# Kernel optimization log

Hardware: AMD Instinct MI355X
Metric: run time of the kernel (lower is better)

## Reference

```python
import jax, jax.numpy as jnp
import numpy as np

W, B, C, H = 1600, 4, 1, 900
DENSITY = 0.03          # fraction of valid radar returns per column
DEPTH_MAX = 80.0        # metric depth range


def setup_inputs() -> dict:
    key = jax.random.key(0)
    k1, k2, k3 = jax.random.split(key, 3)
    radar_depth = jax.random.uniform(k1, (W, B, C, H, 1), jnp.float32) * DEPTH_MAX + 1.0
    radar_mask = jax.random.uniform(k2, (W, B, C, H, 1), jnp.float32) < DENSITY
    radar_patches = jnp.where(radar_mask, radar_depth, 0.0)
    # dense monocular depth estimate, strictly positive (all 'valid')
    mde_out_patches = jax.random.uniform(k3, (W, B, C, H, 1), jnp.float32) * DEPTH_MAX + 1.0
    return {"radar_patches": radar_patches, "mde_out_patches": mde_out_patches}


def _process_column(radar_col, mde_col):
    """Sequentially place valid radar depths of one (w,b) column.

    radar_col, mde_col: [H] float (channel 0 of the column).
    Returns radar_gt column [H].
    Matches torch loop: for each valid radar y (ascending), pick mde row with
    closest depth (argmin |mde - d|, first index on ties); if that slot is
    already occupied, search outward offsets +1,-1,+2,-2,... for an empty slot;
    if none found, overwrite the best slot.
    """
    h = radar_col.shape[0]
    ys = jnp.arange(h)
    mde_valid = mde_col != 0
    has_mde = jnp.any(mde_valid)
    BIG = jnp.float32(1e30)
    KBIG = 4 * h  # sentinel key for occupied slots

    def step(col, y):
        depth = radar_col[y]
        valid = depth != 0
        # per-point argmin over valid mde depths
        diffs = jnp.where(mde_valid, jnp.abs(mde_col - depth), BIG)
        best_y = jnp.where(has_mde, jnp.argmin(diffs), y)
        # outward collision search as a vectorized argmin over a priority key:
        #   best_y itself -> 0; offset o, +dy before -dy -> 2*o + (dy<0)
        occ = col != 0
        dy = ys - best_y
        key = 2 * jnp.abs(dy) + (dy < 0).astype(jnp.int32)
        key = jnp.where(ys == best_y, 0, key)
        key = jnp.where(occ, KBIG, key)
        final_y = jnp.argmin(key)
        # all slots occupied -> fall back to best_y (torch overwrites there)
        final_y = jnp.where(key[final_y] >= KBIG, best_y, final_y)
        new_col = jnp.where(valid, col.at[final_y].set(depth), col)
        return new_col, None

    col, _ = jax.lax.scan(step, jnp.zeros(h, radar_col.dtype), ys)
    return col


def reference(radar_patches, mde_out_patches):
    # channel 0 only is read/written, as in the torch code
    radar0 = radar_patches[:, :, 0, :, 0]   # [W, B, H]
    mde0 = mde_out_patches[:, :, 0, :, 0]   # [W, B, H]
    cols = jax.vmap(jax.vmap(_process_column))(radar0, mde0)  # [W, B, H]
    w, b, h = cols.shape
    c = radar_patches.shape[2]
    radar_gt = jnp.zeros((b, c, h, w), radar_patches.dtype)
    radar_gt = radar_gt.at[:, 0].set(jnp.transpose(cols, (1, 2, 0)))  # [B, H, W]
    return radar_gt
```

## Files before the change

kernel.cpp:

```cpp
#include <hip/hip_runtime.h>
#include <cstdint>
#include <cstddef>

#define WDIM 1600
#define BDIM 4
#define HDIM 900
#define NV4  225
#define QCAP 96
#define KBIG (4 * HDIM)
#define BW   6
#define NWAVE 4

#define DPP_MINF(v, ctrl)                                                  \
    v = fminf(v, __int_as_float(__builtin_amdgcn_update_dpp(               \
            __float_as_int(v), __float_as_int(v), ctrl, 0xf, 0xf, false)))
#define DPP_MINI(v, ctrl)                                                  \
    { int _t = __builtin_amdgcn_update_dpp(v, v, ctrl, 0xf, 0xf, false);   \
      v = _t < v ? _t : v; }

__device__ __forceinline__ float rdlane_f(float v, int l) {
    return __int_as_float(__builtin_amdgcn_readlane(__float_as_int(v), l));
}

__global__ __launch_bounds__(64 * NWAVE, 6) void radar_place_kernel(
    const float* __restrict__ radar, const float* __restrict__ mde,
    float* __restrict__ colout , int direct, float* __restrict__ out)
{
    __shared__ __align__(16) float s_col[NWAVE][HDIM];
    __shared__ float s_qd[NWAVE][QCAP];
    __shared__ int   s_qy[NWAVE][QCAP];

    const int wave = threadIdx.x >> 6;
    const int lane = threadIdx.x & 63;
    const int colid = blockIdx.x * NWAVE + wave;
    const float4* mde4   = (const float4*)mde   + (long)colid * NV4;
    const float4* radar4 = (const float4*)radar + (long)colid * NV4;

    float*  colw = s_col[wave];
    float4* col4 = (float4*)colw;
    float*  qd   = s_qd[wave];
    int*    qy   = s_qy[wave];

    const unsigned long long below = (1ull << lane) - 1ull;

    bool hm = false;
#pragma unroll
    for (int c = 0; c < 4; ++c) {
        int i4 = c * 64 + lane;
        if (i4 < NV4) {
            float4 mv = mde4[i4];
            hm = hm || (mv.x != 0.f) || (mv.y != 0.f) || (mv.z != 0.f) || (mv.w != 0.f);
            col4[i4] = mv;
        }
    }
    const bool has_mde = (__ballot(hm) != 0ull);

    int Q = 0;
#pragma unroll
    for (int c = 0; c < 4; ++c) {
        int i4 = c * 64 + lane;
        bool in = (i4 < NV4);
        float4 rv = in ? radar4[i4] : make_float4(0.f, 0.f, 0.f, 0.f);
        unsigned long long b0 = __ballot(rv.x != 0.f);
        unsigned long long b1 = __ballot(rv.y != 0.f);
        unsigned long long b2 = __ballot(rv.z != 0.f);
        unsigned long long b3 = __ballot(rv.w != 0.f);
        int pos = Q + __popcll(b0 & below) + __popcll(b1 & below)
                    + __popcll(b2 & below) + __popcll(b3 & below);
        int y0 = i4 * 4;
        if (rv.x != 0.f) { if (pos < QCAP) { qd[pos] = rv.x; qy[pos] = y0;     } pos++; }
        if (rv.y != 0.f) { if (pos < QCAP) { qd[pos] = rv.y; qy[pos] = y0 + 1; } pos++; }
        if (rv.z != 0.f) { if (pos < QCAP) { qd[pos] = rv.z; qy[pos] = y0 + 2; } pos++; }
        if (rv.w != 0.f) { if (pos < QCAP) { qd[pos] = rv.w; qy[pos] = y0 + 3; } pos++; }
        Q += __popcll(b0) + __popcll(b1) + __popcll(b2) + __popcll(b3);
    }
    if (Q > QCAP) Q = QCAP;

    float m[15];
    if (lane < 60) {
        int yb = lane * 15;
#pragma unroll
        for (int k = 0; k < 15; ++k) {
            float v = colw[yb + k];
            m[k] = (v != 0.f) ? v : 1e30f;
        }
    } else {
#pragma unroll
        for (int k = 0; k < 15; ++k) m[k] = 1e30f;
    }

    float dq_lo = 0.f, dq_hi = 0.f;
    int   qy_lo = 0,   qy_hi = 0;
    if (lane < Q)      { dq_lo = qd[lane];      qy_lo = qy[lane]; }
    if (lane + 64 < Q) { dq_hi = qd[lane + 64]; qy_hi = qy[lane + 64]; }

#pragma unroll
    for (int c = 0; c < 4; ++c) {
        int i4 = c * 64 + lane;
        if (i4 < NV4) col4[i4] = make_float4(0.f, 0.f, 0.f, 0.f);
    }

    int best_lo = 0, best_hi = 0;
    for (int t = 0; t < Q; t += BW) {
        int idxs[BW];
        float d[BW];
#pragma unroll
        for (int i = 0; i < BW; ++i) {
            int idx = t + i; if (idx >= Q) idx = Q - 1;
            idxs[i] = idx;
            if (idx < 64) d[i] = rdlane_f(dq_lo, idx);
            else          d[i] = rdlane_f(dq_hi, idx - 64);
        }
        float bd[BW], bo[BW];
        int bik[BW];
#pragma unroll
        for (int i = 0; i < BW; ++i) { bd[i] = 3.4e38f; bik[i] = 0; }
#pragma unroll
        for (int k = 0; k < 15; ++k) {
            float mm = m[k];
#pragma unroll
            for (int i = 0; i < BW; ++i) {
                float af = fabsf(mm - d[i]);
                if (af < bd[i]) { bd[i] = af; bik[i] = k; }
            }
        }
#pragma unroll
        for (int i = 0; i < BW; ++i) bo[i] = bd[i];
#pragma unroll
        for (int i = 0; i < BW; ++i) DPP_MINF(bd[i], 0x111);
#pragma unroll
        for (int i = 0; i < BW; ++i) DPP_MINF(bd[i], 0x112);
#pragma unroll
        for (int i = 0; i < BW; ++i) DPP_MINF(bd[i], 0x114);
#pragma unroll
        for (int i = 0; i < BW; ++i) DPP_MINF(bd[i], 0x118);
#pragma unroll
        for (int i = 0; i < BW; ++i) DPP_MINF(bd[i], 0x142);
#pragma unroll
        for (int i = 0; i < BW; ++i) DPP_MINF(bd[i], 0x143);
#pragma unroll
        for (int i = 0; i < BW; ++i) {
            int idx = idxs[i];
            int sb;
            if (has_mde) {
                float gm = rdlane_f(bd[i], 63);
                unsigned long long wm = __ballot(bo[i] == gm);
                int win = __ffsll((long long)wm) - 1;
                int kst = __builtin_amdgcn_readlane(bik[i], win);
                sb = win * 15 + kst;
            } else {
                if (idx < 64) sb = __builtin_amdgcn_readlane(qy_lo, idx);
                else          sb = __builtin_amdgcn_readlane(qy_hi, idx - 64);
            }
            if (idx < 64) { if (lane == idx)      best_lo = sb; }
            else          { if (lane == idx - 64) best_hi = sb; }
        }
    }

    unsigned occ = (lane >= 60) ? 0x7FFFu : 0u;
    int fy_lo = 0, fy_hi = 0;

    auto place_one = [&](int sb) -> int {
        int bl = sb / 15, bk = sb - bl * 15;
        unsigned long long bm = __ballot((occ >> bk) & 1u);
        int fy = sb;
        if ((bm >> bl) & 1ull) {
            int ko = 0x7fffffff, kk = 0;
#pragma unroll
            for (int k = 0; k < 15; ++k) {
                int yy = lane * 15 + k;
                int o = (occ >> k) & 1;
                int dy = yy - sb;
                int ad = dy < 0 ? -dy : dy;
                int key = o ? KBIG : (2 * ad + (dy < 0 ? 1 : 0));
                if (key < ko) { ko = key; kk = k; }
            }
            int km = ko;
            DPP_MINI(km, 0x111); DPP_MINI(km, 0x112); DPP_MINI(km, 0x114);
            DPP_MINI(km, 0x118); DPP_MINI(km, 0x142); DPP_MINI(km, 0x143);
            int gkm = __builtin_amdgcn_readlane(km, 63);
            if (gkm < KBIG) {
                unsigned long long wm2 = __ballot(ko == gkm);
                int w2 = __ffsll((long long)wm2) - 1;
                int k2 = __builtin_amdgcn_readlane(kk, w2);
                fy = w2 * 15 + k2;
            }
        }
        int fl2 = fy / 15, fk2 = fy - (fy / 15) * 15;
        if (lane == fl2) occ |= (1u << fk2);
        return fy;
    };

    int Qlo = Q < 64 ? Q : 64;
    for (int q = 0; q < Qlo; ++q) {
        int fy = place_one(__builtin_amdgcn_readlane(best_lo, q));
        if (lane == q) fy_lo = fy;
    }
    for (int q = 64; q < Q; ++q) {
        int fy = place_one(__builtin_amdgcn_readlane(best_hi, q - 64));
        if (lane == q - 64) fy_hi = fy;
    }

    if (lane < Q)      colw[fy_lo] = dq_lo;
    if (lane + 64 < Q) colw[fy_hi] = dq_hi;

    if (direct) {
        int w_ = colid >> 2, b_ = colid & 3;
#pragma unroll
        for (int c = 0; c < 4; ++c) {
            int i4 = c * 64 + lane;
            if (i4 < NV4) {
                float4 v = col4[i4];
                int y = i4 * 4;
                out[((long)(b_ * HDIM + y + 0)) * WDIM + w_] = v.x;
                out[((long)(b_ * HDIM + y + 1)) * WDIM + w_] = v.y;
                out[((long)(b_ * HDIM + y + 2)) * WDIM + w_] = v.z;
                out[((long)(b_ * HDIM + y + 3)) * WDIM + w_] = v.w;
            }
        }
    } else {
        float4* colout4 = (float4*)colout + (long)colid * NV4;
#pragma unroll
        for (int c = 0; c < 4; ++c) {
            int i4 = c * 64 + lane;
            if (i4 < NV4) colout4[i4] = col4[i4];
        }
    }
}

__global__ __launch_bounds__(256) void transpose_kernel(
    const float* __restrict__ colout, float* __restrict__ out)
{
    __shared__ float tile[32][33];
    const int b  = blockIdx.z;
    const int h0 = blockIdx.x * 32;
    const int w0 = blockIdx.y * 32;
    const int tx = threadIdx.x & 31;
    const int ty = threadIdx.x >> 5;
#pragma unroll
    for (int j = 0; j < 4; ++j) {
        int wl = ty + j * 8;
        int w = w0 + wl;
        int h = h0 + tx;
        float v = 0.0f;
        if (h < HDIM && w < WDIM) v = colout[((long)(w * BDIM + b)) * HDIM + h];
        tile[wl][tx] = v;
    }
    __syncthreads();
#pragma unroll
    for (int j = 0; j < 4; ++j) {
        int hl = ty + j * 8;
        int h = h0 + hl;
        int w = w0 + tx;
        if (h < HDIM && w < WDIM)
            out[((long)(b * HDIM + h)) * WDIM + w] = tile[tx][hl];
    }
}

extern "C" void kernel_launch(void* const* d_in, const int* in_sizes, int n_in,
                              void* d_out, int out_size, void* d_ws, size_t ws_size,
                              hipStream_t stream) {
    const float* radar = (const float*)d_in[0];
    const float* mde   = (const float*)d_in[1];
    float* out = (float*)d_out;
    float* ws  = (float*)d_ws;

    const size_t need = (size_t)WDIM * BDIM * HDIM * sizeof(float);
    const int direct = (ws_size < need) ? 1 : 0;

    hipLaunchKernelGGL(radar_place_kernel,
                       dim3(WDIM * BDIM / NWAVE), dim3(64 * NWAVE), 0, stream,
                       radar, mde, ws, direct, out);

    if (!direct) {
        dim3 g((HDIM + 31) / 32, WDIM / 32, BDIM);
        hipLaunchKernelGGL(transpose_kernel, g, dim3(256), 0, stream, ws, out);
    }
}
```

Baseline: 138.7 us.

## Pack lane/slot/y indices, widen argmin batch, hoist has_mde branch

Raises the number of radar points resolved per argmin batch from 6 to 9 and hoists the has_mde test out of the batch loop. Points beyond 64 are now handled one at a time, and the loaded qy array is dropped from the main path. Best and final slots are packed as (lane, k, y) so the per-placement divides by 15 disappear. The occupancy check becomes a single readlane instead of a ballot. Launch bounds rise to 7 blocks per CU, which tightens the register budget while the batch grows, so spills are a risk.

```diff
diff --git a/kernel.cpp b/kernel.cpp
--- a/kernel.cpp
+++ b/kernel.cpp
@@ -8,7 +8,7 @@
 #define NV4  225
 #define QCAP 96
 #define KBIG (4 * HDIM)
-#define BW   6
+#define BW   9
 #define NWAVE 4
 
 #define DPP_MINF(v, ctrl)                                                  \
@@ -22,7 +22,11 @@
     return __int_as_float(__builtin_amdgcn_readlane(__float_as_int(v), l));
 }
 
-__global__ __launch_bounds__(64 * NWAVE, 6) void radar_place_kernel(
+__device__ __forceinline__ int pack_lky(int l, int k) {
+    return (l << 20) | (k << 16) | (l * 15 + k);
+}
+
+__global__ __launch_bounds__(64 * NWAVE, 7) void radar_place_kernel(
     const float* __restrict__ radar, const float* __restrict__ mde,
     float* __restrict__ colout , int direct, float* __restrict__ out)
 {
@@ -90,9 +94,8 @@
     }
 
     float dq_lo = 0.f, dq_hi = 0.f;
-    int   qy_lo = 0,   qy_hi = 0;
-    if (lane < Q)      { dq_lo = qd[lane];      qy_lo = qy[lane]; }
-    if (lane + 64 < Q) { dq_hi = qd[lane + 64]; qy_hi = qy[lane + 64]; }
+    if (lane < Q)      dq_lo = qd[lane];
+    if (lane + 64 < Q) dq_hi = qd[lane + 64];
 
 #pragma unroll
     for (int c = 0; c < 4; ++c) {
@@ -101,76 +104,101 @@
     }
 
     int best_lo = 0, best_hi = 0;
-    for (int t = 0; t < Q; t += BW) {
-        int idxs[BW];
-        float d[BW];
-#pragma unroll
-        for (int i = 0; i < BW; ++i) {
-            int idx = t + i; if (idx >= Q) idx = Q - 1;
-            idxs[i] = idx;
-            if (idx < 64) d[i] = rdlane_f(dq_lo, idx);
-            else          d[i] = rdlane_f(dq_hi, idx - 64);
-        }
-        float bd[BW], bo[BW];
-        int bik[BW];
-#pragma unroll
-        for (int i = 0; i < BW; ++i) { bd[i] = 3.4e38f; bik[i] = 0; }
-#pragma unroll
-        for (int k = 0; k < 15; ++k) {
-            float mm = m[k];
+    const int Qlo = Q < 64 ? Q : 64;
+
+    if (has_mde) {
+        for (int t = 0; t < Qlo; t += BW) {
+            float d[BW];
 #pragma unroll
             for (int i = 0; i < BW; ++i) {
-                float af = fabsf(mm - d[i]);
-                if (af < bd[i]) { bd[i] = af; bik[i] = k; }
-            }
-        }
-#pragma unroll
-        for (int i = 0; i < BW; ++i) bo[i] = bd[i];
-#pragma unroll
-        for (int i = 0; i < BW; ++i) DPP_MINF(bd[i], 0x111);
-#pragma unroll
-        for (int i = 0; i < BW; ++i) DPP_MINF(bd[i], 0x112);
-#pragma unroll
-        for (int i = 0; i < BW; ++i) DPP_MINF(bd[i], 0x114);
-#pragma unroll
-        for (int i = 0; i < BW; ++i) DPP_MINF(bd[i], 0x118);
-#pragma unroll
-        for (int i = 0; i < BW; ++i) DPP_MINF(bd[i], 0x142);
-#pragma unroll
-        for (int i = 0; i < BW; ++i) DPP_MINF(bd[i], 0x143);
-#pragma unroll
-        for (int i = 0; i < BW; ++i) {
-            int idx = idxs[i];
-            int sb;
-            if (has_mde) {
-                float gm = rdlane_f(bd[i], 63);
-                unsigned long long wm = __ballot(bo[i] == gm);
+                int idx = t + i; if (idx >= Qlo) idx = Qlo - 1;
+                d[i] = rdlane_f(dq_lo, idx);
+            }
+            float bd[BW], bo[BW];
+            int bik[BW];
+#pragma unroll
+            for (int i = 0; i < BW; ++i) { bd[i] = 3.4e38f; bik[i] = 0; }
+#pragma unroll
+            for (int k = 0; k < 15; ++k) {
+                float mm = m[k];
+#pragma unroll
+                for (int i = 0; i < BW; ++i) {
+                    float af = fabsf(mm - d[i]);
+                    if (af < bd[i]) { bd[i] = af; bik[i] = k; }
+                }
+            }
+#pragma unroll
+            for (int i = 0; i < BW; ++i) bo[i] = bd[i];
+#pragma unroll
+            for (int i = 0; i < BW; ++i) DPP_MINF(bd[i], 0x111);
+#pragma unroll
+            for (int i = 0; i < BW; ++i) DPP_MINF(bd[i], 0x112);
+#pragma unroll
+            for (int i = 0; i < BW; ++i) DPP_MINF(bd[i], 0x114);
+#pragma unroll
+            for (int i = 0; i < BW; ++i) DPP_MINF(bd[i], 0x118);
+#pragma unroll
+            for (int i = 0; i < BW; ++i) DPP_MINF(bd[i], 0x142);
+#pragma unroll
+            for (int i = 0; i < BW; ++i) DPP_MINF(bd[i], 0x143);
+#pragma unroll
+            for (int i = 0; i < BW; ++i) {
+                int idx = t + i;
+                if (idx < Qlo) {
+                    float gm = rdlane_f(bd[i], 63);
+                    unsigned long long wm = __ballot(bo[i] == gm);
+                    int win = __ffsll((long long)wm) - 1;
+                    int kst = __builtin_amdgcn_readlane(bik[i], win);
+                    int pk = pack_lky(win, kst);
+                    if (lane == idx) best_lo = pk;
+                }
+            }
+        }
+        if (Q > 64) {
+            for (int t = 64; t < Q; t += 1) {
+                float d0 = rdlane_f(dq_hi, t - 64);
+                float bd0 = 3.4e38f, bo0; int bik0 = 0;
+#pragma unroll
+                for (int k = 0; k < 15; ++k) {
+                    float af = fabsf(m[k] - d0);
+                    if (af < bd0) { bd0 = af; bik0 = k; }
+                }
+                bo0 = bd0;
+                DPP_MINF(bd0, 0x111); DPP_MINF(bd0, 0x112); DPP_MINF(bd0, 0x114);
+                DPP_MINF(bd0, 0x118); DPP_MINF(bd0, 0x142); DPP_MINF(bd0, 0x143);
+                float gm = rdlane_f(bd0, 63);
+                unsigned long long wm = __ballot(bo0 == gm);
                 int win = __ffsll((long long)wm) - 1;
-                int kst = __builtin_amdgcn_readlane(bik[i], win);
-                sb = win * 15 + kst;
-            } else {
-                if (idx < 64) sb = __builtin_amdgcn_readlane(qy_lo, idx);
-                else          sb = __builtin_amdgcn_readlane(qy_hi, idx - 64);
-            }
-            if (idx < 64) { if (lane == idx)      best_lo = sb; }
-            else          { if (lane == idx - 64) best_hi = sb; }
+                int kst = __builtin_amdgcn_readlane(bik0, win);
+                int pk = pack_lky(win, kst);
+                if (lane == t - 64) best_hi = pk;
+            }
+        }
+    } else {
+        for (int q = 0; q < Q; ++q) {
+            int y = qy[q];
+            int l = y / 15, k = y - l * 15;
+            int pk = pack_lky(l, k);
+            if (q < 64) { if (lane == q)      best_lo = pk; }
+            else        { if (lane == q - 64) best_hi = pk; }
         }
     }
 
     unsigned occ = (lane >= 60) ? 0x7FFFu : 0u;
     int fy_lo = 0, fy_hi = 0;
 
-    auto place_one = [&](int sb) -> int {
-        int bl = sb / 15, bk = sb - bl * 15;
-        unsigned long long bm = __ballot((occ >> bk) & 1u);
-        int fy = sb;
-        if ((bm >> bl) & 1ull) {
+    auto place_one = [&](int pk) -> int {
+        int bl = pk >> 20, bk = (pk >> 16) & 15;
+        unsigned po = (unsigned)__builtin_amdgcn_readlane((int)occ, bl);
+        int fpk = pk;
+        if ((po >> bk) & 1u) {
+            int sy = pk & 0xffff;
             int ko = 0x7fffffff, kk = 0;
 #pragma unroll
             for (int k = 0; k < 15; ++k) {
                 int yy = lane * 15 + k;
                 int o = (occ >> k) & 1;
-                int dy = yy - sb;
+                int dy = yy - sy;
                 int ad = dy < 0 ? -dy : dy;
                 int key = o ? KBIG : (2 * ad + (dy < 0 ? 1 : 0));
                 if (key < ko) { ko = key; kk = k; }
@@ -183,26 +211,27 @@
                 unsigned long long wm2 = __ballot(ko == gkm);
                 int w2 = __ffsll((long long)wm2) - 1;
                 int k2 = __builtin_amdgcn_readlane(kk, w2);
-                fy = w2 * 15 + k2;
-            }
-        }
-        int fl2 = fy / 15, fk2 = fy - (fy / 15) * 15;
-        if (lane == fl2) occ |= (1u << fk2);
-        return fy;
+                fpk = pack_lky(w2, k2);
+            }
+        }
+        int fl = fpk >> 20, fk = (fpk >> 16) & 15;
+        if (lane == fl) occ |= (1u << fk);
+        return fpk;
     };
 
-    int Qlo = Q < 64 ? Q : 64;
     for (int q = 0; q < Qlo; ++q) {
-        int fy = place_one(__builtin_amdgcn_readlane(best_lo, q));
-        if (lane == q) fy_lo = fy;
-    }
-    for (int q = 64; q < Q; ++q) {
-        int fy = place_one(__builtin_amdgcn_readlane(best_hi, q - 64));
-        if (lane == q - 64) fy_hi = fy;
-    }
-
-    if (lane < Q)      colw[fy_lo] = dq_lo;
-    if (lane + 64 < Q) colw[fy_hi] = dq_hi;
+        int fpk = place_one(__builtin_amdgcn_readlane(best_lo, q));
+        if (lane == q) fy_lo = fpk;
+    }
+    if (Q > 64) {
+        for (int q = 64; q < Q; ++q) {
+            int fpk = place_one(__builtin_amdgcn_readlane(best_hi, q - 64));
+            if (lane == q - 64) fy_hi = fpk;
+        }
+    }
+
+    if (lane < Q)      colw[fy_lo & 0xffff] = dq_lo;
+    if (lane + 64 < Q) colw[fy_hi & 0xffff] = dq_hi;
 
     if (direct) {
         int w_ = colid >> 2, b_ = colid & 3;
```

Result: no change. 137.5 us (-0.9%).
